# Performance work log

Measured on AMD Instinct MI355X. Metric: run time of the kernel, lower is better.

Reference implementation:

```python
import jax, jax.numpy as jnp
import numpy as np

B, CIN, COUT, H, W = 8, 128, 256, 64, 64
EPS = 1e-5


def conv2d(x, w, b, pad):
    y = jax.lax.conv_general_dilated(
        x, w, window_strides=(1, 1), padding=[(pad, pad), (pad, pad)],
        dimension_numbers=('NCHW', 'OIHW', 'NCHW'))
    return y + b[None, :, None, None]


def deform_sample(x, offset):
    # x: [B,C,H,W], offset: [B,18,H,W] -> sampled: [B,C,9,H,W]
    b, c, h, w = x.shape
    off = offset.reshape(b, 9, 2, h, w)  # (dy, dx) per kernel tap (torchvision v1 order)
    ky = (jnp.arange(9) // 3 - 1).astype(x.dtype)
    kx = (jnp.arange(9) % 3 - 1).astype(x.dtype)
    py = jnp.arange(h, dtype=x.dtype)[None, None, :, None] + ky[None, :, None, None] + off[:, :, 0]
    px = jnp.arange(w, dtype=x.dtype)[None, None, None, :] + kx[None, :, None, None] + off[:, :, 1]
    y0 = jnp.floor(py); x0 = jnp.floor(px)
    fy = py - y0;       fx = px - x0
    xf = x.reshape(b, c, h * w)

    def gather(iy, ix):
        valid = (iy >= 0) & (iy < h) & (ix >= 0) & (ix < w)
        iyc = jnp.clip(iy, 0, h - 1).astype(jnp.int32)
        ixc = jnp.clip(ix, 0, w - 1).astype(jnp.int32)
        idx = (iyc * w + ixc).reshape(b, -1)  # [B, 9*H*W]
        g = jax.vmap(lambda xb, ib: jnp.take(xb, ib, axis=1))(xf, idx)  # [B,C,9HW]
        return g.reshape(b, c, 9, h, w) * valid.astype(x.dtype)[:, None]

    samp = (gather(y0,     x0    ) * ((1 - fy) * (1 - fx))[:, None]
          + gather(y0,     x0 + 1) * ((1 - fy) * fx      )[:, None]
          + gather(y0 + 1, x0    ) * (fy * (1 - fx)      )[:, None]
          + gather(y0 + 1, x0 + 1) * (fy * fx            )[:, None])
    return samp


def setup_inputs():
    key = jax.random.key(0)
    ks = jax.random.split(key, 8)
    return {
        'x':     jax.random.normal(ks[0], (B, CIN, H, W), jnp.float32),
        'w_off': jax.random.normal(ks[1], (18, CIN, 3, 3), jnp.float32) * 0.01,
        'b_off': jnp.zeros((18,), jnp.float32),
        'w_def': jax.random.normal(ks[2], (COUT, CIN, 3, 3), jnp.float32) * 0.03,
        'b_def': jax.random.normal(ks[3], (COUT,), jnp.float32) * 0.01,
        'gamma': jnp.ones((COUT,), jnp.float32),
        'beta':  jnp.zeros((COUT,), jnp.float32),
        'w_sc':  jax.random.normal(ks[4], (COUT, CIN, 1, 1), jnp.float32) * 0.05,
        'b_sc':  jnp.zeros((COUT,), jnp.float32),
    }


def reference(x, w_off, b_off, w_def, b_def, gamma, beta, w_sc, b_sc):
    offset = conv2d(x, w_off, b_off, pad=1)                 # [B,18,H,W]
    samp = deform_sample(x, offset)                         # [B,C,9,H,W]
    out = jnp.einsum('bckhw,ock->bohw', samp, w_def.reshape(COUT, CIN, 9))
    out = out + b_def[None, :, None, None]
    # BatchNorm2d (training mode: batch statistics)
    mean = out.mean(axis=(0, 2, 3))
    var = out.var(axis=(0, 2, 3))
    out = (out - mean[None, :, None, None]) * jax.lax.rsqrt(var + EPS)[None, :, None, None]
    out = out * gamma[None, :, None, None] + beta[None, :, None, None]
    out = out + conv2d(x, w_sc, b_sc, pad=0)                # residual shortcut (1x1)
    return jax.nn.relu(out)
```

## Files before the change

kernel.cpp:

```cpp
#include <hip/hip_runtime.h>

typedef __attribute__((ext_vector_type(8))) short bf16x8;
typedef __attribute__((ext_vector_type(4))) float f32x4;

__device__ __forceinline__ float bf2f(unsigned short u) {
  return __uint_as_float(((unsigned int)u) << 16);
}
__device__ __forceinline__ unsigned short f2bf(float f) {
  unsigned int u = __float_as_uint(f);
  u += 0x7fffu + ((u >> 16) & 1u);
  return (unsigned short)(u >> 16);
}

constexpr size_t OFF_XPAD = 0;
constexpr size_t SZ_XPAD  = (size_t)8 * 66 * 66 * 128 * 2;
constexpr size_t OFF_WB   = OFF_XPAD + SZ_XPAD;
constexpr size_t SZ_WB    = (size_t)9 * 16 * 256 * 8 * 2;
constexpr size_t OFF_WS2  = OFF_WB + SZ_WB;
constexpr size_t SZ_WS2   = (size_t)16 * 256 * 8 * 2;
constexpr size_t OFF_WO   = OFF_WS2 + SZ_WS2;
constexpr size_t SZ_WO    = (size_t)9 * 16 * 32 * 8 * 2;
constexpr size_t OFF_YM   = OFF_WO + SZ_WO;
constexpr size_t SZ_YM    = (size_t)512 * 512 * 32 * 2;
constexpr size_t OFF_SR   = OFF_YM + SZ_YM;
constexpr size_t SZ_SR    = (size_t)8 * 256 * 2 * 4;


__global__ __launch_bounds__(256) void k_prep(const float* __restrict__ x,
                                              unsigned short* __restrict__ xp,
                                              const float* __restrict__ wdef,
                                              const float* __restrict__ wsc,
                                              const float* __restrict__ woff,
                                              unsigned short* __restrict__ wB,
                                              unsigned short* __restrict__ wS,
                                              unsigned short* __restrict__ wO,
                                              float* __restrict__ statsRaw) {
  int t = threadIdx.x;
  if (blockIdx.x == 690) {
    for (int i = t; i < 4096; i += 256) statsRaw[i] = 0.f;
    return;
  }
  if (blockIdx.x >= 512) {
    int base = ((blockIdx.x - 512) * 256 + t) * 8;
    unsigned short w8[8];
    if (base < 294912) {
      int n = (base >> 3) & 255, kb = (base >> 11) & 15, tap = base >> 15;
#pragma unroll
      for (int j = 0; j < 8; ++j)
        w8[j] = f2bf(wdef[((size_t)n * 128 + kb * 8 + j) * 9 + tap]);
      *(bf16x8*)(wB + base) = *(const bf16x8*)w8;
    } else if (base < 327680) {
      int i0 = base - 294912;
      int n = (i0 >> 3) & 255, kb = i0 >> 11;
#pragma unroll
      for (int j = 0; j < 8; ++j)
        w8[j] = f2bf(wsc[(size_t)n * 128 + kb * 8 + j]);
      *(bf16x8*)(wS + i0) = *(const bf16x8*)w8;
    } else {
      int i0 = base - 327680;
      int n = (i0 >> 3) & 31, kb = (i0 >> 8) & 15, tap = i0 >> 12;
#pragma unroll
      for (int j = 0; j < 8; ++j)
        w8[j] = f2bf(n < 18 ? woff[((size_t)n * 128 + kb * 8 + j) * 9 + tap] : 0.f);
      *(bf16x8*)(wO + i0) = *(const bf16x8*)w8;
    }
    return;
  }
  int blk = blockIdx.x;
  int b = blk & 7, h = blk >> 3;
  __shared__ unsigned short xt[128 * 68];
  {
    unsigned short* base = xp + (size_t)b * 66 * 66 * 128;
    ushort4 z4 = {0, 0, 0, 0};
    if (t < 64) {
      int col = (t >> 5) ? 65 : 0;
      int i = t & 31;
      *(ushort4*)(base + ((size_t)(h + 1) * 66 + col) * 128 + i * 4) = z4;
    }
    if (h == 0) {
      for (int i = t; i < 2112; i += 256) {
        *(ushort4*)(base + (size_t)i * 4) = z4;
        *(ushort4*)(base + (size_t)65 * 66 * 128 + (size_t)i * 4) = z4;
      }
    }
  }
  {
#pragma unroll
    for (int i4 = 0; i4 < 8; ++i4) {
      int idx = t + i4 * 256;
      int row = idx >> 4, col = (idx & 15) * 4;
      float4 f = *(const float4*)&x[(((size_t)b * 128 + row) * 64 + h) * 64 + col];
      ushort4 u4;
      u4.x = f2bf(f.x); u4.y = f2bf(f.y); u4.z = f2bf(f.z); u4.w = f2bf(f.w);
      *(ushort4*)&xt[row * 68 + col] = u4;
    }
  }
  __syncthreads();
  {
    int w = t & 63, cg = t >> 6;
    unsigned short tmp[32];
#pragma unroll
    for (int i = 0; i < 32; ++i) tmp[i] = xt[(cg * 32 + i) * 68 + w];
    unsigned short* dst = xp + ((size_t)(b * 66 + h + 1) * 66 + (w + 1)) * 128 + cg * 32;
#pragma unroll
    for (int i8 = 0; i8 < 4; ++i8)
      *(bf16x8*)(dst + i8 * 8) = *(const bf16x8*)&tmp[i8 * 8];
  }
}

__global__ __launch_bounds__(512, 4) void k_main(const unsigned short* __restrict__ xp,
                                                 const unsigned short* __restrict__ wB,
                                                 const unsigned short* __restrict__ wO,
                                                 const float* __restrict__ boff,
                                                 const float* __restrict__ bdef,
                                                 unsigned short* __restrict__ ymain,
                                                 float* __restrict__ statsRaw) {
  int blk = blockIdx.x;
  int b = blk & 7, h = blk >> 3;
  int t = threadIdx.x;
  int lane = t & 63, wid = t >> 6;
  int m = lane & 15, quad = lane >> 4;
  __shared__ __align__(16) unsigned short At[2][64 * 136];
  __shared__ float offsL[9][64][2];

  if (wid < 4) {
    f32x4 a0 = {0.f, 0.f, 0.f, 0.f}, a1 = {0.f, 0.f, 0.f, 0.f};
    int px = wid * 16 + m;
    const unsigned short* xbase = xp + ((size_t)(b * 66 + h) * 66 + px) * 128 + quad * 8;
    for (int tap = 0; tap < 9; ++tap) {
      const unsigned short* arow = xbase + ((tap / 3) * 66 + (tap % 3)) * 128;
#pragma unroll
      for (int kk = 0; kk < 4; ++kk) {
        bf16x8 a = *(const bf16x8*)(arow + kk * 32);
        const unsigned short* bb = wO + (size_t)(tap * 16 + kk * 4 + quad) * 256;
        bf16x8 b0 = *(const bf16x8*)(bb + m * 8);
        bf16x8 b1 = *(const bf16x8*)(bb + (16 + m) * 8);
        a0 = __builtin_amdgcn_mfma_f32_16x16x32_bf16(a, b0, a0, 0, 0, 0);
        a1 = __builtin_amdgcn_mfma_f32_16x16x32_bf16(a, b1, a1, 0, 0, 0);
      }
    }
#pragma unroll
    for (int r = 0; r < 4; ++r) {
      int pxs = wid * 16 + quad * 4 + r;
      offsL[m >> 1][pxs][m & 1] = a0[r] + boff[m];
      if (m < 2) offsL[8][pxs][m] = a1[r] + boff[16 + m];
    }
  }

  f32x4 acc[4][2];
#pragma unroll
  for (int i = 0; i < 4; ++i)
#pragma unroll
    for (int j = 0; j < 2; ++j) acc[i][j] = (f32x4){0.f, 0.f, 0.f, 0.f};

  int px_s = t >> 3, sub = t & 7;
  const unsigned short* xb_base = xp + (size_t)b * 66 * 66 * 128;
  int nb = wid * 32;

  bf16x8 Breg[4][2];
  auto loadB = [&](int tap) {
#pragma unroll
    for (int kk = 0; kk < 4; ++kk)
#pragma unroll
      for (int ns = 0; ns < 2; ++ns)
        Breg[kk][ns] = *(const bf16x8*)(wB + ((size_t)(tap * 16 + kk * 4 + quad) * 256 + nb + ns * 16 + m) * 8);
  };

  auto sample_prep = [&](int tap, float* wgt, const unsigned short** p) {
    float2 ov = *(const float2*)&offsL[tap][px_s][0];
    int ky = tap / 3 - 1, kx = tap % 3 - 1;
    float py = (float)(h + ky) + ov.x;
    float pxf = (float)(px_s + kx) + ov.y;
    float y0f = floorf(py), x0f = floorf(pxf);
    float fy = py - y0f, fx = pxf - x0f;
    int iy0 = (int)y0f, ix0 = (int)x0f;
#pragma unroll
    for (int j = 0; j < 4; ++j) {
      int iy = iy0 + (j >> 1), ix = ix0 + (j & 1);
      float wy = (j >> 1) ? fy : 1.f - fy;
      float wx = (j & 1) ? fx : 1.f - fx;
      bool valid = (iy >= 0) && (iy < 64) && (ix >= 0) && (ix < 64);
      int iyc = min(max(iy, 0), 63), ixc = min(max(ix, 0), 63);
      wgt[j] = valid ? wy * wx : 0.f;
      p[j] = xb_base + ((size_t)(iyc + 1) * 66 + (ixc + 1)) * 128 + sub * 8;
    }
  };
  auto load_g1 = [&](const unsigned short** p, int g, bf16x8* v) {
#pragma unroll
    for (int j = 0; j < 4; ++j)
      v[j] = *(const bf16x8*)(p[j] + g * 64);
  };
  auto store_g1 = [&](unsigned short* dst, int g, const float* wgt, bf16x8* v) {
    bf16x8 o;
#pragma unroll
    for (int j = 0; j < 8; ++j) {
      float s = fmaf(wgt[0], bf2f((unsigned short)v[0][j]),
                fmaf(wgt[1], bf2f((unsigned short)v[1][j]),
                fmaf(wgt[2], bf2f((unsigned short)v[2][j]),
                     wgt[3] * bf2f((unsigned short)v[3][j]))));
      o[j] = (short)f2bf(s);
    }
    *(bf16x8*)(dst + g * 64) = o;
  };
  auto mfma_half = [&](const unsigned short* buf, int kk0) {
#pragma unroll
    for (int kk = kk0; kk < kk0 + 2; ++kk) {
      bf16x8 af[4];
#pragma unroll
      for (int ms = 0; ms < 4; ++ms)
        af[ms] = *(const bf16x8*)(buf + (ms * 16 + m) * 136 + kk * 32 + quad * 8);
#pragma unroll
      for (int ns = 0; ns < 2; ++ns)
#pragma unroll
        for (int ms = 0; ms < 4; ++ms)
          acc[ms][ns] = __builtin_amdgcn_mfma_f32_16x16x32_bf16(af[ms], Breg[kk][ns], acc[ms][ns], 0, 0, 0);
    }
  };

  loadB(0);
  __syncthreads();
  {
    float wgt[4]; const unsigned short* p[4]; bf16x8 v0[4], v1[4];
    sample_prep(0, wgt, p);
    unsigned short* dst = &At[0][px_s * 136 + sub * 8];
    load_g1(p, 0, v0); load_g1(p, 1, v1);
    store_g1(dst, 0, wgt, v0); store_g1(dst, 1, wgt, v1);
  }
#pragma unroll
  for (int tap = 0; tap < 9; ++tap) {
    __syncthreads();
    const unsigned short* cur = At[tap & 1];
    unsigned short* dst = &At[(tap + 1) & 1][px_s * 136 + sub * 8];
    if (tap < 8) {
      float wgt[4]; const unsigned short* p[4]; bf16x8 v0[4], v1[4];
      sample_prep(tap + 1, wgt, p);
      load_g1(p, 0, v0);
      load_g1(p, 1, v1);
      mfma_half(cur, 0);
      store_g1(dst, 0, wgt, v0);
      mfma_half(cur, 2);
      loadB(tap + 1);
      store_g1(dst, 1, wgt, v1);
    } else {
      mfma_half(cur, 0);
      mfma_half(cur, 2);
    }
  }

#pragma unroll
  for (int ns = 0; ns < 2; ++ns) {
    int n = nb + ns * 16 + m;
    float bias = bdef[n];
    float s = 0.f, q = 0.f;
#pragma unroll
    for (int ms = 0; ms < 4; ++ms)
#pragma unroll
      for (int r = 0; r < 4; ++r) {
        float v = acc[ms][ns][r] + bias;
        acc[ms][ns][r] = v;
        s += v;
        q += v * v;
      }
    s += __shfl_xor(s, 16); s += __shfl_xor(s, 32);
    q += __shfl_xor(q, 16); q += __shfl_xor(q, 32);
    if (quad == 0) {
      atomicAdd(&statsRaw[((size_t)b * 256 + n) * 2 + 0], s);
      atomicAdd(&statsRaw[((size_t)b * 256 + n) * 2 + 1], q);
    }
  }
  {
    unsigned short yfrag[32];
#pragma unroll
    for (int ns = 0; ns < 2; ++ns)
#pragma unroll
      for (int ms = 0; ms < 4; ++ms)
#pragma unroll
        for (int r = 0; r < 4; ++r)
          yfrag[ns * 16 + ms * 4 + r] = f2bf(acc[ms][ns][r]);
    unsigned short* dst = ymain + (size_t)blk * 16384 + t * 8;
#pragma unroll
    for (int k = 0; k < 4; ++k)
      __builtin_nontemporal_store(*(const bf16x8*)&yfrag[k * 8], (bf16x8*)(dst + k * 4096));
  }
}

__global__ __launch_bounds__(256, 4) void k_final(const unsigned short* __restrict__ xp,
                                                  const unsigned short* __restrict__ wS,
                                                  const unsigned short* __restrict__ ymain,
                                                  const float* __restrict__ statsRaw,
                                                  const float* __restrict__ gamma,
                                                  const float* __restrict__ beta,
                                                  const float* __restrict__ bsc,
                                                  float* __restrict__ out) {
  int blk = blockIdx.x;
  int b = blk & 7, rem = blk >> 3, h = rem >> 1, chalf = rem & 1;
  int t = threadIdx.x;
  int lane = t & 63, wid = t >> 6;
  int m = lane & 15, quad = lane >> 4;
  __shared__ __align__(16) float tr[128 * 68];
  __shared__ float sAB[256];
  if (t < 128) {
    int ch = chalf * 128 + t;
    float s = 0.f, q = 0.f;
#pragma unroll
    for (int i = 0; i < 8; ++i) {
      float2 pq = *(const float2*)&statsRaw[((size_t)i * 256 + ch) * 2];
      s += pq.x;
      q += pq.y;
    }
    float mean = s * (1.f / 32768.f);
    float var = q * (1.f / 32768.f) - mean * mean;
    float inv = rsqrtf(var + 1e-5f);
    float A = gamma[ch] * inv;
    sAB[t] = A;
    sAB[128 + t] = beta[ch] - mean * A;
  }
  f32x4 accS[4][2];
#pragma unroll
  for (int i = 0; i < 4; ++i)
#pragma unroll
    for (int j = 0; j < 2; ++j) accS[i][j] = (f32x4){0.f, 0.f, 0.f, 0.f};
  const unsigned short* xrow = xp + ((size_t)(b * 66 + h + 1) * 66 + 1) * 128;
  int nbl = wid * 32;
  int nbg = chalf * 128 + nbl;
#pragma unroll
  for (int kk = 0; kk < 4; ++kk) {
    bf16x8 af[4];
#pragma unroll
    for (int ms = 0; ms < 4; ++ms)
      af[ms] = *(const bf16x8*)(xrow + (ms * 16 + m) * 128 + kk * 32 + quad * 8);
#pragma unroll
    for (int ns = 0; ns < 2; ++ns) {
      bf16x8 bfr = *(const bf16x8*)(wS + ((size_t)(kk * 4 + quad) * 256 + nbg + ns * 16 + m) * 8);
#pragma unroll
      for (int ms = 0; ms < 4; ++ms)
        accS[ms][ns] = __builtin_amdgcn_mfma_f32_16x16x32_bf16(af[ms], bfr, accS[ms][ns], 0, 0, 0);
    }
  }
  bf16x8 yf[4];
  {
    int blk_main = h * 8 + b;
    int t_main = (chalf * 4 + wid) * 64 + lane;
    const unsigned short* ysrc = ymain + (size_t)blk_main * 16384 + t_main * 8;
#pragma unroll
    for (int k = 0; k < 4; ++k)
      yf[k] = *(const bf16x8*)(ysrc + k * 4096);
  }
  __syncthreads();
#pragma unroll
  for (int ns = 0; ns < 2; ++ns) {
    int nl = nbl + ns * 16 + m;
    float A = sAB[nl], Bc = sAB[128 + nl], bs = bsc[chalf * 128 + nl];
#pragma unroll
    for (int ms = 0; ms < 4; ++ms)
#pragma unroll
      for (int r = 0; r < 4; ++r) {
        int e = ns * 16 + ms * 4 + r;
        float y = bf2f((unsigned short)yf[e >> 3][e & 7]);
        float v = fmaf(y, A, Bc) + accS[ms][ns][r] + bs;
        tr[nl * 68 + ms * 16 + quad * 4 + r] = fmaxf(v, 0.f);
      }
  }
  __syncthreads();
  {
    int q4 = t & 3, nl0 = t >> 2;
#pragma unroll
    for (int it = 0; it < 2; ++it) {
      int nl = it * 64 + nl0;
      float* orow = out + ((size_t)(b * 256 + chalf * 128 + nl) * 64 + h) * 64 + q4 * 16;
      const float* lrow = &tr[nl * 68 + q4 * 16];
#pragma unroll
      for (int i4 = 0; i4 < 4; ++i4)
        *(f32x4*)(orow + i4 * 4) = *(const f32x4*)(lrow + i4 * 4);
    }
  }
}

extern "C" void kernel_launch(void* const* d_in, const int* in_sizes, int n_in,
                              void* d_out, int out_size, void* d_ws, size_t ws_size,
                              hipStream_t stream) {
  const float* x     = (const float*)d_in[0];
  const float* w_off = (const float*)d_in[1];
  const float* b_off = (const float*)d_in[2];
  const float* w_def = (const float*)d_in[3];
  const float* b_def = (const float*)d_in[4];
  const float* gamma = (const float*)d_in[5];
  const float* beta  = (const float*)d_in[6];
  const float* w_sc  = (const float*)d_in[7];
  const float* b_sc  = (const float*)d_in[8];
  float* out = (float*)d_out;

  char* ws = (char*)d_ws;
  unsigned short* xpad  = (unsigned short*)(ws + OFF_XPAD);
  unsigned short* wB    = (unsigned short*)(ws + OFF_WB);
  unsigned short* wS    = (unsigned short*)(ws + OFF_WS2);
  unsigned short* wO    = (unsigned short*)(ws + OFF_WO);
  unsigned short* ymain = (unsigned short*)(ws + OFF_YM);
  float* statsRaw       = (float*)(ws + OFF_SR);

  k_prep<<<691, 256, 0, stream>>>(x, xpad, w_def, w_sc, w_off, wB, wS, wO, statsRaw);
  k_main<<<512, 512, 0, stream>>>(xpad, wB, wO, b_off, b_def, ymain, statsRaw);
  k_final<<<1024, 256, 0, stream>>>(xpad, wS, ymain, statsRaw, gamma, beta, b_sc, out);
}
```

Measured before the change: 156.0 us.

## Prefetch deformable gather two taps ahead and pad LDS row stride

Restructures the per-tap pipeline so the bilinear gather loads for tap+2 are issued into a double-buffered register slot while the current tap's MFMAs and the next tap's blend run, deepening latency hiding of the global gathers. The LDS tile row stride changes from 136 to 140 elements to alter bank mapping for the A-fragment reads. Launch bounds drop from 4 to 2 blocks per CU so the compiler has room for the extra live registers, trading occupancy for more in-flight loads per wave.

```diff
diff --git a/kernel.cpp b/kernel.cpp
--- a/kernel.cpp
+++ b/kernel.cpp
@@ -108,7 +108,7 @@
   }
 }
 
-__global__ __launch_bounds__(512, 4) void k_main(const unsigned short* __restrict__ xp,
+__global__ __launch_bounds__(512, 2) void k_main(const unsigned short* __restrict__ xp,
                                                  const unsigned short* __restrict__ wB,
                                                  const unsigned short* __restrict__ wO,
                                                  const float* __restrict__ boff,
@@ -120,7 +120,7 @@
   int t = threadIdx.x;
   int lane = t & 63, wid = t >> 6;
   int m = lane & 15, quad = lane >> 4;
-  __shared__ __align__(16) unsigned short At[2][64 * 136];
+  __shared__ __align__(16) unsigned short At[2][64 * 140];
   __shared__ float offsL[9][64][2];
 
   if (wid < 4) {
@@ -166,6 +166,9 @@
         Breg[kk][ns] = *(const bf16x8*)(wB + ((size_t)(tap * 16 + kk * 4 + quad) * 256 + nb + ns * 16 + m) * 8);
   };
 
+  bf16x8 vbuf[2][8];
+  float wbuf[2][4];
+
   auto sample_prep = [&](int tap, float* wgt, const unsigned short** p) {
     float2 ov = *(const float2*)&offsL[tap][px_s][0];
     int ky = tap / 3 - 1, kx = tap % 3 - 1;
@@ -185,19 +188,22 @@
       p[j] = xb_base + ((size_t)(iyc + 1) * 66 + (ixc + 1)) * 128 + sub * 8;
     }
   };
-  auto load_g1 = [&](const unsigned short** p, int g, bf16x8* v) {
-#pragma unroll
-    for (int j = 0; j < 4; ++j)
-      v[j] = *(const bf16x8*)(p[j] + g * 64);
+  auto prep_issue = [&](int tap, int slot) {
+    const unsigned short* p[4];
+    sample_prep(tap, wbuf[slot], p);
+#pragma unroll
+    for (int j = 0; j < 4; ++j) vbuf[slot][j] = *(const bf16x8*)(p[j]);
+#pragma unroll
+    for (int j = 0; j < 4; ++j) vbuf[slot][4 + j] = *(const bf16x8*)(p[j] + 64);
   };
-  auto store_g1 = [&](unsigned short* dst, int g, const float* wgt, bf16x8* v) {
+  auto blend_half = [&](unsigned short* dst, int slot, int g) {
     bf16x8 o;
 #pragma unroll
     for (int j = 0; j < 8; ++j) {
-      float s = fmaf(wgt[0], bf2f((unsigned short)v[0][j]),
-                fmaf(wgt[1], bf2f((unsigned short)v[1][j]),
-                fmaf(wgt[2], bf2f((unsigned short)v[2][j]),
-                     wgt[3] * bf2f((unsigned short)v[3][j]))));
+      float s = fmaf(wbuf[slot][0], bf2f((unsigned short)vbuf[slot][g * 4 + 0][j]),
+                fmaf(wbuf[slot][1], bf2f((unsigned short)vbuf[slot][g * 4 + 1][j]),
+                fmaf(wbuf[slot][2], bf2f((unsigned short)vbuf[slot][g * 4 + 2][j]),
+                     wbuf[slot][3] * bf2f((unsigned short)vbuf[slot][g * 4 + 3][j]))));
       o[j] = (short)f2bf(s);
     }
     *(bf16x8*)(dst + g * 64) = o;
@@ -208,7 +214,7 @@
       bf16x8 af[4];
 #pragma unroll
       for (int ms = 0; ms < 4; ++ms)
-        af[ms] = *(const bf16x8*)(buf + (ms * 16 + m) * 136 + kk * 32 + quad * 8);
+        af[ms] = *(const bf16x8*)(buf + (ms * 16 + m) * 140 + kk * 32 + quad * 8);
 #pragma unroll
       for (int ns = 0; ns < 2; ++ns)
 #pragma unroll
@@ -220,27 +226,24 @@
   loadB(0);
   __syncthreads();
   {
-    float wgt[4]; const unsigned short* p[4]; bf16x8 v0[4], v1[4];
-    sample_prep(0, wgt, p);
-    unsigned short* dst = &At[0][px_s * 136 + sub * 8];
-    load_g1(p, 0, v0); load_g1(p, 1, v1);
-    store_g1(dst, 0, wgt, v0); store_g1(dst, 1, wgt, v1);
+    prep_issue(0, 0);
+    unsigned short* dst0 = &At[0][px_s * 140 + sub * 8];
+    blend_half(dst0, 0, 0);
+    blend_half(dst0, 0, 1);
+    prep_issue(1, 1);
   }
 #pragma unroll
   for (int tap = 0; tap < 9; ++tap) {
     __syncthreads();
     const unsigned short* cur = At[tap & 1];
-    unsigned short* dst = &At[(tap + 1) & 1][px_s * 136 + sub * 8];
+    unsigned short* dst = &At[(tap + 1) & 1][px_s * 140 + sub * 8];
     if (tap < 8) {
-      float wgt[4]; const unsigned short* p[4]; bf16x8 v0[4], v1[4];
-      sample_prep(tap + 1, wgt, p);
-      load_g1(p, 0, v0);
-      load_g1(p, 1, v1);
+      if (tap < 7) prep_issue(tap + 2, tap & 1);
       mfma_half(cur, 0);
-      store_g1(dst, 0, wgt, v0);
+      blend_half(dst, (tap + 1) & 1, 0);
       mfma_half(cur, 2);
+      blend_half(dst, (tap + 1) & 1, 1);
       loadB(tap + 1);
-      store_g1(dst, 1, wgt, v1);
     } else {
       mfma_half(cur, 0);
       mfma_half(cur, 2);
```

After: 209.3 us. +34.2%, slower.
